# Kernel tuning notes

Measured on AMD Instinct MI355X. Metric: run time of the kernel, lower is better.

Reference implementation:

```python
import jax, jax.numpy as jnp
import numpy as np

GROUP = 8          # weight_group_size
QMAX = 7.0         # 2**(4-1)-1, narrow-range symmetric int4
EPS = 1e-8


def quant_dequant(w):
    """Per-group (size 8, along in_features) symmetric int4 quant-dequant.
    w: [out, in] -> dequantized [out, in]."""
    O, I = w.shape
    wg = w.reshape(O, I // GROUP, GROUP)
    scale = jnp.max(jnp.abs(wg), axis=-1, keepdims=True) / QMAX  # [O, I/G, 1]
    scale = jnp.maximum(scale, EPS)
    q = jnp.clip(jnp.round(wg / scale), -QMAX, QMAX)
    return (q * scale).reshape(O, I)


def setup_inputs() -> dict:
    key = jax.random.key(0)
    kx, kw, kb = jax.random.split(key, 3)
    tokens, din, dout = 8192, 4096, 4096
    x = jax.random.normal(kx, (tokens, din), dtype=jnp.float32)
    weight = jax.random.normal(kw, (dout, din), dtype=jnp.float32) * 0.02
    bias = jax.random.normal(kb, (dout,), dtype=jnp.float32) * 0.01
    return {"x": x, "weight": weight, "bias": bias}


def reference(x, weight, bias):
    w_deq = quant_dequant(weight)                 # [out, in]
    return jnp.dot(x, w_deq.T) + bias             # [tokens, out]
```

## Files before the change

kernel.cpp:

```cpp
#include <hip/hip_runtime.h>
#include <hip/hip_bf16.h>
#include <stdint.h>

typedef __attribute__((ext_vector_type(8))) __bf16 bf16x8;
typedef __attribute__((ext_vector_type(4))) float f32x4;
typedef __attribute__((ext_vector_type(8))) unsigned short ushort8;

typedef const void __attribute__((address_space(1))) gv_t;
typedef void __attribute__((address_space(3))) lv_t;

#define GL16(g, l) __builtin_amdgcn_global_load_lds((gv_t*)(g), (lv_t*)(l), 16, 0, 0)

__device__ __forceinline__ unsigned short f2bf(float f) {
    unsigned int u = __float_as_uint(f);
    u += 0x7fffu + ((u >> 16) & 1u);
    return (unsigned short)(u >> 16);
}

__global__ void __launch_bounds__(256) qdq_weight(const float* __restrict__ w,
                                                  unsigned short* __restrict__ wb,
                                                  int n_groups) {
    int g = blockIdx.x * 256 + threadIdx.x;
    if (g >= n_groups) return;
    const float4* p = (const float4*)w + (size_t)g * 2;
    float4 v0 = p[0], v1 = p[1];
    float t[8] = {v0.x, v0.y, v0.z, v0.w, v1.x, v1.y, v1.z, v1.w};
    float amax = 0.0f;
#pragma unroll
    for (int j = 0; j < 8; ++j) amax = fmaxf(amax, fabsf(t[j]));
    float scale = fmaxf(amax / 7.0f, 1e-8f);
    ushort8 o;
#pragma unroll
    for (int j = 0; j < 8; ++j) {
        float q = rintf(t[j] / scale);
        q = fminf(fmaxf(q, -7.0f), 7.0f);
        o[j] = f2bf(q * scale);
    }
    *((ushort8*)wb + g) = o;
}

__global__ void __launch_bounds__(256) cvt_bf16(const float* __restrict__ x,
                                                unsigned short* __restrict__ xb,
                                                int n8) {
    int i = blockIdx.x * 256 + threadIdx.x;
    if (i >= n8) return;
    const float4* p = (const float4*)x + (size_t)i * 2;
    float4 v0 = p[0], v1 = p[1];
    ushort8 o;
    o[0] = f2bf(v0.x); o[1] = f2bf(v0.y); o[2] = f2bf(v0.z); o[3] = f2bf(v0.w);
    o[4] = f2bf(v1.x); o[5] = f2bf(v1.y); o[6] = f2bf(v1.z); o[7] = f2bf(v1.w);
    *((ushort8*)xb + i) = o;
}

#define BM 256
#define BN 256
#define BK 64

#define MFMA_Q(qm, qn, AF, BF)                                                 \
    __builtin_amdgcn_s_setprio(1);                                             \
    _Pragma("unroll")                                                          \
    for (int mi = 0; mi < 4; ++mi)                                             \
        _Pragma("unroll")                                                      \
        for (int ni = 0; ni < 2; ++ni)                                         \
            _Pragma("unroll")                                                  \
            for (int ks = 0; ks < 2; ++ks)                                     \
                acc[(qm) * 4 + mi][(qn) * 2 + ni] =                            \
                    __builtin_amdgcn_mfma_f32_16x16x32_bf16(                   \
                        AF[mi][ks], BF[ni][ks],                                \
                        acc[(qm) * 4 + mi][(qn) * 2 + ni], 0, 0, 0);           \
    __builtin_amdgcn_s_setprio(0);

#define STAGE_A(b, h, kk)                                                      \
    {                                                                          \
        GL16(gA + (size_t)((h) * 64 + srow) * K + (kk) + schunk,               \
             &sA[b][h][0] + sldso);                                            \
        GL16(gA + (size_t)((h) * 64 + 128 + srow) * K + (kk) + schunk,         \
             &sA[b][h][64 * BK] + sldso);                                      \
    }
#define STAGE_B(b, h, kk)                                                      \
    {                                                                          \
        GL16(gB + (size_t)((h) * 32 + brow) * K + (kk) + schunk,               \
             &sB[b][h][0] + sldso);                                            \
        GL16(gB + (size_t)((h) * 32 + 128 + brow) * K + (kk) + schunk,         \
             &sB[b][h][64 * BK] + sldso);                                      \
    }

#define READ_A(dst, b, h)                                                      \
    _Pragma("unroll")                                                          \
    for (int mi = 0; mi < 4; ++mi) {                                           \
        const int s_ = (wr * 64 + mi * 16 + lr) * BK;                          \
        dst[mi][0] = *(const bf16x8*)&sA[b][h][s_ + e0];                       \
        dst[mi][1] = *(const bf16x8*)&sA[b][h][s_ + e1];                       \
    }
#define READ_B(dst, b, h)                                                      \
    _Pragma("unroll")                                                          \
    for (int ni = 0; ni < 2; ++ni) {                                           \
        const int s_ = (bcol + ni * 16 + lr) * BK;                             \
        dst[ni][0] = *(const bf16x8*)&sB[b][h][s_ + e0];                       \
        dst[ni][1] = *(const bf16x8*)&sB[b][h][s_ + e1];                       \
    }

#define BAR()  asm volatile("s_barrier" ::: "memory")
#define VM(n)  asm volatile("s_waitcnt vmcnt(" #n ")" ::: "memory")

__global__ void __launch_bounds__(512, 2)
gemm256(const unsigned short* __restrict__ A,
        const unsigned short* __restrict__ B,
        const float* __restrict__ bias,
        float* __restrict__ C,
        int M, int N, int K) {
    __shared__ unsigned short sA[2][2][128 * BK];
    __shared__ unsigned short sB[2][2][128 * BK];

    const int t  = threadIdx.x;
    const int w  = t >> 6;
    const int ln = t & 63;
    const int lr = ln & 15;
    const int lk = ln >> 4;
    const int wr = w >> 2;
    const int wc = w & 3;
    const int bcol = (wc >> 1) * 64 + (wc & 1) * 32;

    const int nbn = N / BN;
    const int bid = blockIdx.x;
    const int swz = ((int)gridDim.x & 7) ? bid
                  : ((bid & 7) * ((int)gridDim.x >> 3) + (bid >> 3));
    const int m0 = (swz / nbn) * BM;
    const int n0 = (swz % nbn) * BN;

    const unsigned short* gA = A + (size_t)m0 * K;
    const unsigned short* gB = B + (size_t)n0 * K;

    const int srow   = t >> 3;
    const int brow   = (srow & 31) + ((srow >> 5) << 6);
    const int schunk = (((t & 7) ^ (srow & 7)) << 3);
    const int sldso  = (w * 8) * BK;

    const int sw = (lr & 7) << 3;
    const int e0 = (lk * 8) ^ sw;
    const int e1 = (32 + lk * 8) ^ sw;

    f32x4 acc[8][4];
#pragma unroll
    for (int i = 0; i < 8; ++i)
#pragma unroll
        for (int j = 0; j < 4; ++j)
            acc[i][j] = (f32x4)(0.0f);

    const int NT = K / BK;
    const int J  = NT / 2;

    bf16x8 a0f[4][2], a1f[4][2], b0f[2][2], b1f[2][2];

    STAGE_A(0, 0, 0);
    STAGE_B(0, 0, 0);
    STAGE_B(0, 1, 0);
    STAGE_A(0, 1, 0);
    STAGE_A(1, 0, BK);
    STAGE_B(1, 0, BK);
    STAGE_B(1, 1, BK);
    VM(8);
    BAR();
    READ_A(a0f, 0, 0);

    for (int it = 0; it < J; ++it) {
        const int t0 = 2 * it;
        const int k1 = (t0 + 1) * BK;
        int k2 = (t0 + 2) * BK;  if (k2 >= K) k2 = 0;
        int k3 = (t0 + 3) * BK;  if (k3 >= K) k3 = 0;

        READ_B(b0f, 0, 0); READ_B(b1f, 0, 1);
        STAGE_A(1, 1, k1);
        MFMA_Q(0, 0, a0f, b0f);
        VM(8); BAR();

        READ_A(a1f, 0, 1);
        STAGE_A(0, 0, k2);
        MFMA_Q(0, 1, a0f, b1f);
        VM(8); BAR();

        READ_A(a0f, 1, 0);
        STAGE_B(0, 0, k2);
        MFMA_Q(1, 1, a1f, b1f);
        VM(8); BAR();

        STAGE_B(0, 1, k2);
        MFMA_Q(1, 0, a1f, b0f);
        VM(8); BAR();

        READ_B(b0f, 1, 0); READ_B(b1f, 1, 1);
        STAGE_A(0, 1, k2);
        MFMA_Q(0, 0, a0f, b0f);
        VM(8); BAR();

        READ_A(a1f, 1, 1);
        STAGE_A(1, 0, k3);
        MFMA_Q(0, 1, a0f, b1f);
        VM(8); BAR();

        READ_A(a0f, 0, 0);
        STAGE_B(1, 0, k3);
        MFMA_Q(1, 1, a1f, b1f);
        VM(8); BAR();

        STAGE_B(1, 1, k3);
        MFMA_Q(1, 0, a1f, b0f);
        VM(8); BAR();
    }

#pragma unroll
    for (int j = 0; j < 4; ++j) {
        const int n = n0 + wc * 64 + (j >> 1) * 32 + (j & 1) * 16 + lr;
        const float bv = bias[n];
#pragma unroll
        for (int i = 0; i < 8; ++i) {
            const int m = m0 + wr * 128 + (i >> 2) * 64 + (i & 3) * 16 + lk * 4;
            f32x4 v = acc[i][j];
            C[(size_t)(m + 0) * N + n] = v[0] + bv;
            C[(size_t)(m + 1) * N + n] = v[1] + bv;
            C[(size_t)(m + 2) * N + n] = v[2] + bv;
            C[(size_t)(m + 3) * N + n] = v[3] + bv;
        }
    }
}

extern "C" void kernel_launch(void* const* d_in, const int* in_sizes, int n_in,
                              void* d_out, int out_size, void* d_ws, size_t ws_size,
                              hipStream_t stream) {
    const float* x    = (const float*)d_in[0];
    const float* wgt  = (const float*)d_in[1];
    const float* bias = (const float*)d_in[2];
    float* out        = (float*)d_out;

    const int dout = in_sizes[2];
    const int din  = in_sizes[1] / dout;
    const int M    = in_sizes[0] / din;
    const int N    = dout, K = din;

    unsigned short* xb = (unsigned short*)d_ws;
    unsigned short* wb = xb + (size_t)M * K;

    const int ng_w = (N * K) / 8;
    qdq_weight<<<(ng_w + 255) / 256, 256, 0, stream>>>(wgt, wb, ng_w);

    const int n8_x = (M * K) / 8;
    cvt_bf16<<<(n8_x + 255) / 256, 256, 0, stream>>>(x, xb, n8_x);

    const int nwg = (M / BM) * (N / BN);
    gemm256<<<nwg, 512, 0, stream>>>(xb, wb, bias, out, M, N, K);
}
```

Before: 307.8 us.

## Restructure GEMM main loop into phased LDS-read/stage/MFMA schedule with sched barriers

```diff
diff --git a/kernel.cpp b/kernel.cpp
--- a/kernel.cpp
+++ b/kernel.cpp
@@ -100,8 +100,23 @@
         dst[ni][1] = *(const bf16x8*)&sB[b][h][s_ + e1];                       \
     }
 
-#define BAR()  asm volatile("s_barrier" ::: "memory")
-#define VM(n)  asm volatile("s_waitcnt vmcnt(" #n ")" ::: "memory")
+#define BAR_()     asm volatile("s_barrier" ::: "memory")
+#define VM_(n)     asm volatile("s_waitcnt vmcnt(" #n ")" ::: "memory")
+#define LGKM_(n)   asm volatile("s_waitcnt lgkmcnt(" #n ")" ::: "memory")
+#define SCHEDBAR() __builtin_amdgcn_sched_barrier(0)
+
+#define PHASE(RDS, STG, QM, QN, AF, BF, HINT, VMQ)                             \
+    {                                                                          \
+        RDS;                                                                   \
+        STG;                                                                   \
+        HINT;                                                                  \
+        BAR_();                                                                \
+        LGKM_(0);                                                              \
+        SCHEDBAR();                                                            \
+        MFMA_Q(QM, QN, AF, BF);                                                \
+        VMQ;                                                                   \
+        BAR_();                                                                \
+    }
 
 __global__ void __launch_bounds__(512, 2)
 gemm256(const unsigned short* __restrict__ A,
@@ -154,14 +169,12 @@
 
     STAGE_A(0, 0, 0);
     STAGE_B(0, 0, 0);
+    STAGE_A(0, 1, 0);
     STAGE_B(0, 1, 0);
-    STAGE_A(0, 1, 0);
     STAGE_A(1, 0, BK);
     STAGE_B(1, 0, BK);
-    STAGE_B(1, 1, BK);
-    VM(8);
-    BAR();
-    READ_A(a0f, 0, 0);
+    VM_(4);
+    BAR_();
 
     for (int it = 0; it < J; ++it) {
         const int t0 = 2 * it;
@@ -169,43 +182,21 @@
         int k2 = (t0 + 2) * BK;  if (k2 >= K) k2 = 0;
         int k3 = (t0 + 3) * BK;  if (k3 >= K) k3 = 0;
 
-        READ_B(b0f, 0, 0); READ_B(b1f, 0, 1);
-        STAGE_A(1, 1, k1);
-        MFMA_Q(0, 0, a0f, b0f);
-        VM(8); BAR();
-
-        READ_A(a1f, 0, 1);
-        STAGE_A(0, 0, k2);
-        MFMA_Q(0, 1, a0f, b1f);
-        VM(8); BAR();
-
-        READ_A(a0f, 1, 0);
-        STAGE_B(0, 0, k2);
-        MFMA_Q(1, 1, a1f, b1f);
-        VM(8); BAR();
-
-        STAGE_B(0, 1, k2);
-        MFMA_Q(1, 0, a1f, b0f);
-        VM(8); BAR();
-
-        READ_B(b0f, 1, 0); READ_B(b1f, 1, 1);
-        STAGE_A(0, 1, k2);
-        MFMA_Q(0, 0, a0f, b0f);
-        VM(8); BAR();
-
-        READ_A(a1f, 1, 1);
-        STAGE_A(1, 0, k3);
-        MFMA_Q(0, 1, a0f, b1f);
-        VM(8); BAR();
-
-        READ_A(a0f, 0, 0);
-        STAGE_B(1, 0, k3);
-        MFMA_Q(1, 1, a1f, b1f);
-        VM(8); BAR();
-
-        STAGE_B(1, 1, k3);
-        MFMA_Q(1, 0, a1f, b0f);
-        VM(8); BAR();
+        PHASE(READ_A(a0f, 0, 0); READ_B(b0f, 0, 0),
+              STAGE_A(1, 1, k1), 0, 0, a0f, b0f, LGKM_(8), );
+        PHASE(READ_A(a1f, 0, 1),
+              STAGE_B(1, 1, k1), 1, 0, a1f, b0f, , );
+        PHASE(READ_B(b1f, 0, 1),
+              STAGE_A(0, 0, k2), 1, 1, a1f, b1f, , );
+        PHASE(, STAGE_B(0, 0, k2), 0, 1, a0f, b1f, , VM_(4));
+
+        PHASE(READ_A(a0f, 1, 0); READ_B(b0f, 1, 0),
+              STAGE_A(0, 1, k2), 0, 0, a0f, b0f, LGKM_(8), );
+        PHASE(READ_A(a1f, 1, 1),
+              STAGE_B(0, 1, k2), 1, 0, a1f, b0f, , );
+        PHASE(READ_B(b1f, 1, 1),
+              STAGE_A(1, 0, k3), 1, 1, a1f, b1f, , );
+        PHASE(, STAGE_B(1, 0, k3), 0, 1, a0f, b1f, , VM_(4));
     }
 
 #pragma unroll
```

Result: faster. 296.8 us (-3.6%).
